# Optimization experiments

Hardware: AMD Instinct MI355X
Metric: run time of the kernel (lower is better)

The kernel has to match this reference:

```python
import jax, jax.numpy as jnp
import numpy as np

N = 100_000          # nodes
E = 3_200_000        # edges (avg degree 32)
EMB = 16             # item embedding dim
IN = EMB + 1         # concat(embed, scalar feature)
HID = 32             # GAT hidden size
NEMB = 1000          # embedding vocab
SLOPE = 0.2          # GATConv leaky_relu negative slope


def setup_inputs() -> dict:
    key = jax.random.key(0)
    ks = jax.random.split(key, 24)
    g = lambda k, shape, fan: jax.random.normal(k, shape, dtype=jnp.float32) * (1.0 / np.sqrt(fan))
    inp = {
        "x_ids": jax.random.randint(ks[0], (N,), 0, NEMB, dtype=jnp.int32),
        "x_feat": jax.random.normal(ks[1], (N, 1), dtype=jnp.float32),
        "src": jax.random.randint(ks[2], (E,), 0, N, dtype=jnp.int32),
        "dst": jax.random.randint(ks[3], (E,), 0, N, dtype=jnp.int32),
        "edge_attr": jax.random.normal(ks[4], (E, 1), dtype=jnp.float32),
        # embedding table
        "emb": g(ks[5], (NEMB, EMB), EMB),
        # GATConv 1 (in=17, out=32, heads=1, edge_dim=1)
        "W1": g(ks[6], (IN, HID), IN),
        "a_s1": g(ks[7], (HID,), HID),
        "a_d1": g(ks[8], (HID,), HID),
        "We1": g(ks[9], (1, HID), 1),
        "a_e1": g(ks[10], (HID,), HID),
        "b1": jnp.zeros((HID,), jnp.float32),
        # GATConv 2 (in=32, out=32)
        "W2": g(ks[11], (HID, HID), HID),
        "a_s2": g(ks[12], (HID,), HID),
        "a_d2": g(ks[13], (HID,), HID),
        "We2": g(ks[14], (1, HID), 1),
        "a_e2": g(ks[15], (HID,), HID),
        "b2": jnp.zeros((HID,), jnp.float32),
        # final linear (32 -> 1)
        "lin_w": g(ks[16], (HID, 1), HID),
        "lin_b": jnp.zeros((1,), jnp.float32),
    }
    return inp


def _gat_conv(x, src, dst, eattr, W, a_s, a_d, We, a_e, b):
    """PyG GATConv (heads=1, concat=True) with edge features, self-loops already added."""
    h = x @ W                                   # [N, HID]
    alpha_src = h @ a_s                         # [N]
    alpha_dst = h @ a_d                         # [N]
    alpha_edge = (eattr @ We) @ a_e             # [E']
    alpha = jax.nn.leaky_relu(alpha_src[src] + alpha_dst[dst] + alpha_edge, SLOPE)
    # segment softmax over incoming edges of each dst node
    m = jax.ops.segment_max(alpha, dst, num_segments=N)
    ex = jnp.exp(alpha - m[dst])
    denom = jax.ops.segment_sum(ex, dst, num_segments=N)
    coef = ex / (denom[dst] + 1e-16)
    out = jax.ops.segment_sum(coef[:, None] * h[src], dst, num_segments=N)
    return out + b


def reference(x_ids, x_feat, src, dst, edge_attr, emb,
              W1, a_s1, a_d1, We1, a_e1, b1,
              W2, a_s2, a_d2, We2, a_e2, b2,
              lin_w, lin_b):
    # embedding lookup + concat scalar feature -> [N, 17]
    x = jnp.concatenate([emb[x_ids], x_feat], axis=1)

    # add self-loops once; self-loop edge_attr = mean of incoming edge attrs (fill_value='mean')
    loop = jnp.arange(N, dtype=src.dtype)
    deg = jax.ops.segment_sum(jnp.ones((E,), x.dtype), dst, num_segments=N)
    loop_attr = jax.ops.segment_sum(edge_attr, dst, num_segments=N) / jnp.maximum(deg, 1.0)[:, None]
    src2 = jnp.concatenate([src, loop])
    dst2 = jnp.concatenate([dst, loop])
    ea2 = jnp.concatenate([edge_attr, loop_attr], axis=0)

    x = _gat_conv(x, src2, dst2, ea2, W1, a_s1, a_d1, We1, a_e1, b1)
    x = jax.nn.relu(x)  # dropout is identity in eval mode
    x = _gat_conv(x, src2, dst2, ea2, W2, a_s2, a_d2, We2, a_e2, b2)
    return x @ lin_w + lin_b  # [N, 1]
```

## Files before the change

### kernel.cpp

```cpp
#include <hip/hip_runtime.h>
#include <hip/hip_fp16.h>

#define NN 100000
#define EE 3200000
#define SLOPE 0.2f

#define BKN 128
constexpr int NBK = (NN + BKN - 1) / BKN;
#define CAP 4544
#define EPB 4096
constexpr int NBB = (EE + EPB - 1) / EPB;
constexpr int NBT = (NN + 255) / 256;
#define SUBN 1344

__global__ void k_fat(const int* __restrict__ src, const int* __restrict__ dst,
                      const float* __restrict__ ea, int* __restrict__ cnt,
                      int2* __restrict__ stage,
                      const int* __restrict__ ids, const float* __restrict__ feat,
                      const float* __restrict__ emb, const float* __restrict__ W,
                      const float* __restrict__ avs, const float* __restrict__ avd,
                      __half* __restrict__ h, float* __restrict__ as_,
                      float* __restrict__ ad_) {
    __shared__ int hst[NBK];
    __shared__ int scl[NBK];
    __shared__ int gdel[NBK];
    __shared__ int aux[256];
    __shared__ int2 rec[EPB];
    __shared__ int addr[EPB];
    int t = threadIdx.x;
    if (blockIdx.x < NBB) {
        int base = blockIdx.x * EPB;
        int nedge = min(EPB, EE - base);
        for (int i = t; i < NBK; i += 256) hst[i] = 0;
        __syncthreads();
        int ds[16], ss[16]; float es[16];
#pragma unroll
        for (int j = 0; j < 16; j++) {
            int e = base + j * 256 + t;
            bool v = e < EE;
            ds[j] = v ? dst[e] : -1;
            ss[j] = v ? src[e] : 0;
            es[j] = v ? ea[e] : 0.f;
            if (v) atomicAdd(&hst[ds[j] >> 7], 1);
        }
        __syncthreads();
        int i0 = t * 4;
        int v0 = (i0 + 0 < NBK) ? hst[i0 + 0] : 0;
        int v1 = (i0 + 1 < NBK) ? hst[i0 + 1] : 0;
        int v2 = (i0 + 2 < NBK) ? hst[i0 + 2] : 0;
        int v3 = (i0 + 3 < NBK) ? hst[i0 + 3] : 0;
        int tsum = v0 + v1 + v2 + v3;
        aux[t] = tsum;
        __syncthreads();
        for (int off = 1; off < 256; off <<= 1) {
            int x = (t >= off) ? aux[t - off] : 0;
            __syncthreads();
            aux[t] += x;
            __syncthreads();
        }
        int ex = aux[t] - tsum;
        if (i0 + 0 < NBK) scl[i0 + 0] = ex;
        if (i0 + 1 < NBK) scl[i0 + 1] = ex + v0;
        if (i0 + 2 < NBK) scl[i0 + 2] = ex + v0 + v1;
        if (i0 + 3 < NBK) scl[i0 + 3] = ex + v0 + v1 + v2;
        __syncthreads();
        for (int i = t; i < NBK; i += 256) {
            int hh = hst[i];
            int g = hh ? atomicAdd(&cnt[i], hh) : 0;
            gdel[i] = (g + i * CAP) - scl[i];
        }
        __syncthreads();
#pragma unroll
        for (int j = 0; j < 16; j++) {
            if (ds[j] >= 0) {
                int bk = ds[j] >> 7;
                int pos = atomicAdd(&scl[bk], 1);
                int gpos = pos + gdel[bk];
                rec[pos] = make_int2(ss[j] | ((ds[j] & 127) << 17), __float_as_int(es[j]));
                addr[pos] = (gpos - bk * CAP < CAP) ? gpos : -1;
            }
        }
        __syncthreads();
        for (int i = t; i < nedge; i += 256) {
            int a = addr[i];
            if (a >= 0) stage[a] = rec[i];
        }
    } else {
        int n = (blockIdx.x - NBB) * 256 + t;
        if (n >= NN) return;
        float hv[32];
#pragma unroll
        for (int j = 0; j < 32; j++) hv[j] = 0.f;
        int id = ids[n];
        const float4* e4 = (const float4*)(emb + (size_t)id * 16);
#pragma unroll
        for (int k4 = 0; k4 < 4; k4++) {
            float4 xv = e4[k4];
            const float* wr = W + k4 * 4 * 32;
#pragma unroll
            for (int j = 0; j < 32; j++)
                hv[j] += xv.x * wr[j] + xv.y * wr[32 + j] + xv.z * wr[64 + j] + xv.w * wr[96 + j];
        }
        float f = feat[n];
#pragma unroll
        for (int j = 0; j < 32; j++) hv[j] += f * W[16 * 32 + j];
        float s = 0.f, d = 0.f;
#pragma unroll
        for (int j = 0; j < 32; j++) { s += hv[j] * avs[j]; d += hv[j] * avd[j]; }
        as_[n] = s;
        ad_[n] = d;
        __half2 tmp[16];
#pragma unroll
        for (int q = 0; q < 16; q++) tmp[q] = __floats2half2_rn(hv[2 * q], hv[2 * q + 1]);
        uint4* dst4 = (uint4*)(h + (size_t)n * 32);
        const uint4* s4 = (const uint4*)tmp;
#pragma unroll
        for (int q = 0; q < 4; q++) dst4[q] = s4[q];
    }
}

template <bool FINAL>
__global__ __launch_bounds__(256, 6) void k_agg(
    const int* __restrict__ cnt, const int2* __restrict__ stage,
    const __half* __restrict__ h, const float* __restrict__ as_,
    const float* __restrict__ ad_, const float* __restrict__ We,
    const float* __restrict__ ae, const float* __restrict__ bias,
    const float* __restrict__ W2, const float* __restrict__ avs2,
    const float* __restrict__ avd2, __half* __restrict__ hout,
    float* __restrict__ as2, float* __restrict__ ad2,
    const float* __restrict__ lw, const float* __restrict__ lb,
    float* __restrict__ out) {
    __shared__ int2 ebuf[SUBN];
    __shared__ int2 xb[4][64];
    __shared__ float w2s[1024];
    __shared__ float xrow[4][32];
    __shared__ int ldeg[32];
    __shared__ float esum[32];
    __shared__ int starts[32];
    __shared__ int lcur[32];
    __shared__ int cnts[32];
    __shared__ float means[32];
    int t = threadIdx.x;
    int b2 = blockIdx.x;
    int b = b2 >> 2, q = b2 & 3;
    int nbase = b * BKN + q * 32;
    int npb = min(32, NN - nbase);
    if (npb <= 0) return;
    int lane = t & 63;
    int wid = t >> 6;
    int g = lane >> 4;
    int cp = (lane & 15) * 2;
    int comp = lane & 31;
    float ce = We[comp] * ae[comp];
#pragma unroll
    for (int off = 1; off < 32; off <<= 1) ce += __shfl_xor(ce, off);

    if (t < 32) { ldeg[t] = 0; esum[t] = 0.f; }
    if (!FINAL)
        for (int i = t; i < 1024; i += 256) w2s[i] = W2[i];
    __syncthreads();
    int c = min(cnt[b], CAP);
    const int2* ep = stage + (size_t)b * CAP;
    for (int i = t; i < c; i += 256) {
        int2 e = ep[i];
        int dl = (e.x >> 17) & 127;
        if ((dl >> 5) == q) {
            atomicAdd(&ldeg[dl & 31], 1);
            atomicAdd(&esum[dl & 31], __int_as_float(e.y));
        }
    }
    __syncthreads();
    if (t < 64) {
        int l = lane;
        int dv = (l < npb) ? ldeg[l] + 1 : 0;
        int v = dv;
#pragma unroll
        for (int off = 1; off < 32; off <<= 1) {
            int x = __shfl_up(v, off);
            if (lane >= off) v += x;
        }
        if (l < 32) {
            int st = v - dv;
            starts[l] = st;
            lcur[l] = st;
            cnts[l] = dv;
            means[l] = esum[l] / fmaxf((float)ldeg[l], 1.0f);
        }
    }
    __syncthreads();
    for (int i = t; i < c; i += 256) {
        int2 e = ep[i];
        int dl = (e.x >> 17) & 127;
        if ((dl >> 5) == q) {
            int pos = atomicAdd(&lcur[dl & 31], 1);
            if (pos < SUBN) ebuf[pos] = make_int2(e.x & 0x1FFFF, e.y);
        }
    }
    __syncthreads();
    if (t < npb) {
        int p = lcur[t];
        if (p < SUBN) ebuf[p] = make_int2(nbase + t, __float_as_int(means[t]));
    }
    __syncthreads();

    for (int i2 = 0; i2 < 8; i2++) {
        int n = wid * 8 + i2;
        if (n >= npb) break;
        int gn = nbase + n;
        int base2 = starts[n];
        int cn = cnts[n];
        if (base2 >= SUBN) cn = 0;
        else if (cn > SUBN - base2) cn = SUBN - base2;
        float adn = ad_[gn];
        float2 acc0 = {0.f, 0.f}, acc1 = {0.f, 0.f}, acc2 = {0.f, 0.f}, acc3 = {0.f, 0.f};
        float exs = 0.f;
        for (int cb = 0; cb < cn; cb += 64) {
            int idx = cb + lane;
            bool val = idx < cn;
            int2 e = ebuf[base2 + (val ? idx : 0)];
            float a = as_[e.x] + adn + ce * __int_as_float(e.y);
            a = (a >= 0.f) ? a : SLOPE * a;
            float ex = val ? __expf(a) : 0.f;
            exs += ex;
            xb[wid][lane] = make_int2(e.x << 5, __float_as_int(ex));
            int m = min(cn - cb, 64);
            for (int j = 0; j < m; j += 16) {
                int2 p0 = xb[wid][j + g];
                int2 p1 = xb[wid][j + 4 + g];
                int2 p2 = xb[wid][j + 8 + g];
                int2 p3 = xb[wid][j + 12 + g];
                float2 h0 = __half22float2(*(const __half2*)(h + p0.x + cp));
                float2 h1 = __half22float2(*(const __half2*)(h + p1.x + cp));
                float2 h2 = __half22float2(*(const __half2*)(h + p2.x + cp));
                float2 h3 = __half22float2(*(const __half2*)(h + p3.x + cp));
                float w0 = __int_as_float(p0.y), w1 = __int_as_float(p1.y);
                float w2 = __int_as_float(p2.y), w3 = __int_as_float(p3.y);
                acc0.x += w0 * h0.x; acc0.y += w0 * h0.y;
                acc1.x += w1 * h1.x; acc1.y += w1 * h1.y;
                acc2.x += w2 * h2.x; acc2.y += w2 * h2.y;
                acc3.x += w3 * h3.x; acc3.y += w3 * h3.y;
            }
        }
        float2 acc;
        acc.x = (acc0.x + acc1.x) + (acc2.x + acc3.x);
        acc.y = (acc0.y + acc1.y) + (acc2.y + acc3.y);
        acc.x += __shfl_xor(acc.x, 16); acc.y += __shfl_xor(acc.y, 16);
        acc.x += __shfl_xor(acc.x, 32); acc.y += __shfl_xor(acc.y, 32);
#pragma unroll
        for (int off = 1; off < 64; off <<= 1) exs += __shfl_xor(exs, off);
        float inv = 1.0f / (exs + 1e-16f);
        float ox = acc.x * inv + bias[cp];
        float oy = acc.y * inv + bias[cp + 1];
        if (FINAL) {
            float y = ox * lw[cp] + oy * lw[cp + 1];
#pragma unroll
            for (int off = 1; off < 16; off <<= 1) y += __shfl_xor(y, off);
            if (lane == 0) out[gn] = y + lb[0];
        } else {
            ox = fmaxf(ox, 0.f);
            oy = fmaxf(oy, 0.f);
            if (lane < 16) { xrow[wid][cp] = ox; xrow[wid][cp + 1] = oy; }
            float hx = 0.f, hy = 0.f;
#pragma unroll
            for (int k = 0; k < 32; k++) {
                float xk = xrow[wid][k];
                hx += xk * w2s[k * 32 + cp];
                hy += xk * w2s[k * 32 + cp + 1];
            }
            float ps = hx * avs2[cp] + hy * avs2[cp + 1];
            float pd = hx * avd2[cp] + hy * avd2[cp + 1];
#pragma unroll
            for (int off = 1; off < 16; off <<= 1) {
                ps += __shfl_xor(ps, off);
                pd += __shfl_xor(pd, off);
            }
            if (lane == 0) { as2[gn] = ps; ad2[gn] = pd; }
            if (lane < 16)
                *(__half2*)(hout + ((size_t)gn << 5) + cp) = __floats2half2_rn(hx, hy);
        }
    }
}


extern "C" void kernel_launch(void* const* d_in, const int* in_sizes, int n_in,
                              void* d_out, int out_size, void* d_ws, size_t ws_size,
                              hipStream_t stream) {
    const int* x_ids = (const int*)d_in[0];
    const float* x_feat = (const float*)d_in[1];
    const int* src = (const int*)d_in[2];
    const int* dst = (const int*)d_in[3];
    const float* eattr = (const float*)d_in[4];
    const float* emb = (const float*)d_in[5];
    const float* W1 = (const float*)d_in[6];
    const float* a_s1 = (const float*)d_in[7];
    const float* a_d1 = (const float*)d_in[8];
    const float* We1 = (const float*)d_in[9];
    const float* a_e1 = (const float*)d_in[10];
    const float* b1 = (const float*)d_in[11];
    const float* W2 = (const float*)d_in[12];
    const float* a_s2 = (const float*)d_in[13];
    const float* a_d2 = (const float*)d_in[14];
    const float* We2 = (const float*)d_in[15];
    const float* a_e2 = (const float*)d_in[16];
    const float* b2 = (const float*)d_in[17];
    const float* lin_w = (const float*)d_in[18];
    const float* lin_b = (const float*)d_in[19];

    char* p = (char*)d_ws;
    auto alloc = [&](size_t bytes) {
        void* r = (void*)p;
        p += (bytes + 255) & ~(size_t)255;
        return r;
    };
    int* cnt = (int*)alloc(NBK * 4);
    float* asb1 = (float*)alloc(NN * 4);
    float* adb1 = (float*)alloc(NN * 4);
    float* asb2 = (float*)alloc(NN * 4);
    float* adb2 = (float*)alloc(NN * 4);
    __half* h1 = (__half*)alloc((size_t)NN * 32 * 2);
    __half* h2 = (__half*)alloc((size_t)NN * 32 * 2);
    int2* stage = (int2*)alloc((size_t)NBK * CAP * 8);
    (void)ws_size; (void)in_sizes; (void)n_in; (void)out_size;

    hipMemsetAsync(cnt, 0, NBK * 4, stream);

    k_fat<<<NBB + NBT, 256, 0, stream>>>(src, dst, eattr, cnt, stage,
                                         x_ids, x_feat, emb, W1, a_s1, a_d1,
                                         h1, asb1, adb1);
    k_agg<false><<<NBK * 4, 256, 0, stream>>>(cnt, stage, h1, asb1, adb1,
                                              We1, a_e1, b1,
                                              W2, a_s2, a_d2, h2, asb2, adb2,
                                              nullptr, nullptr, nullptr);
    k_agg<true><<<NBK * 4, 256, 0, stream>>>(cnt, stage, h2, asb2, adb2,
                                             We2, a_e2, b2,
                                             nullptr, nullptr, nullptr,
                                             nullptr, nullptr, nullptr,
                                             lin_w, lin_b, (float*)d_out);
}
```

Measured before the change: 349.3 us.

## Bucket edges per 32-node sub-block so aggregation reads only its own edges

The edge binning pass now buckets edges by dst>>5 (3125 buckets of 32 nodes) instead of dst>>7. Each aggregation block therefore reads only its own bucket rather than scanning a 128-node bucket four times and discarding three quarters of the entries. The per-block shared histogram grows to 3328 entries and the edges handled per binning block drop to 1792, which means more binning blocks and more global atomics on cnt. Launch bounds are raised to 8 waves, and the code now assumes NN divides evenly by 32 and that each bucket holds at most 1344 edges.

```diff
diff --git a/kernel.cpp b/kernel.cpp
--- a/kernel.cpp
+++ b/kernel.cpp
@@ -5,10 +5,11 @@
 #define EE 3200000
 #define SLOPE 0.2f
 
-#define BKN 128
-constexpr int NBK = (NN + BKN - 1) / BKN;
-#define CAP 4544
-#define EPB 4096
+#define SBN 32
+constexpr int NSB = NN / SBN;
+#define NSBP 3328
+#define CAPS 1344
+#define EPB 1792
 constexpr int NBB = (EE + EPB - 1) / EPB;
 constexpr int NBT = (NN + 255) / 256;
 #define SUBN 1344
@@ -21,9 +22,9 @@
                       const float* __restrict__ avs, const float* __restrict__ avd,
                       __half* __restrict__ h, float* __restrict__ as_,
                       float* __restrict__ ad_) {
-    __shared__ int hst[NBK];
-    __shared__ int scl[NBK];
-    __shared__ int gdel[NBK];
+    __shared__ int hst[NSBP];
+    __shared__ int scl[NSBP];
+    __shared__ int gdel[NSBP];
     __shared__ int aux[256];
     __shared__ int2 rec[EPB];
     __shared__ int addr[EPB];
@@ -31,25 +32,24 @@
     if (blockIdx.x < NBB) {
         int base = blockIdx.x * EPB;
         int nedge = min(EPB, EE - base);
-        for (int i = t; i < NBK; i += 256) hst[i] = 0;
-        __syncthreads();
-        int ds[16], ss[16]; float es[16];
-#pragma unroll
-        for (int j = 0; j < 16; j++) {
+        for (int i = t; i < NSBP; i += 256) hst[i] = 0;
+        __syncthreads();
+        int ds[7], ss[7]; float es[7];
+#pragma unroll
+        for (int j = 0; j < 7; j++) {
             int e = base + j * 256 + t;
             bool v = e < EE;
             ds[j] = v ? dst[e] : -1;
             ss[j] = v ? src[e] : 0;
             es[j] = v ? ea[e] : 0.f;
-            if (v) atomicAdd(&hst[ds[j] >> 7], 1);
-        }
-        __syncthreads();
-        int i0 = t * 4;
-        int v0 = (i0 + 0 < NBK) ? hst[i0 + 0] : 0;
-        int v1 = (i0 + 1 < NBK) ? hst[i0 + 1] : 0;
-        int v2 = (i0 + 2 < NBK) ? hst[i0 + 2] : 0;
-        int v3 = (i0 + 3 < NBK) ? hst[i0 + 3] : 0;
-        int tsum = v0 + v1 + v2 + v3;
+            if (v) atomicAdd(&hst[ds[j] >> 5], 1);
+        }
+        __syncthreads();
+        int i0 = t * 13;
+        int vv[13];
+        int tsum = 0;
+#pragma unroll
+        for (int j = 0; j < 13; j++) { vv[j] = hst[i0 + j]; tsum += vv[j]; }
         aux[t] = tsum;
         __syncthreads();
         for (int off = 1; off < 256; off <<= 1) {
@@ -59,25 +59,23 @@
             __syncthreads();
         }
         int ex = aux[t] - tsum;
-        if (i0 + 0 < NBK) scl[i0 + 0] = ex;
-        if (i0 + 1 < NBK) scl[i0 + 1] = ex + v0;
-        if (i0 + 2 < NBK) scl[i0 + 2] = ex + v0 + v1;
-        if (i0 + 3 < NBK) scl[i0 + 3] = ex + v0 + v1 + v2;
-        __syncthreads();
-        for (int i = t; i < NBK; i += 256) {
+#pragma unroll
+        for (int j = 0; j < 13; j++) { scl[i0 + j] = ex; ex += vv[j]; }
+        __syncthreads();
+        for (int i = t; i < NSB; i += 256) {
             int hh = hst[i];
             int g = hh ? atomicAdd(&cnt[i], hh) : 0;
-            gdel[i] = (g + i * CAP) - scl[i];
-        }
-        __syncthreads();
-#pragma unroll
-        for (int j = 0; j < 16; j++) {
+            gdel[i] = (g + i * CAPS) - scl[i];
+        }
+        __syncthreads();
+#pragma unroll
+        for (int j = 0; j < 7; j++) {
             if (ds[j] >= 0) {
-                int bk = ds[j] >> 7;
+                int bk = ds[j] >> 5;
                 int pos = atomicAdd(&scl[bk], 1);
                 int gpos = pos + gdel[bk];
-                rec[pos] = make_int2(ss[j] | ((ds[j] & 127) << 17), __float_as_int(es[j]));
-                addr[pos] = (gpos - bk * CAP < CAP) ? gpos : -1;
+                rec[pos] = make_int2(ss[j] | ((ds[j] & 31) << 17), __float_as_int(es[j]));
+                addr[pos] = (gpos - bk * CAPS < CAPS) ? gpos : -1;
             }
         }
         __syncthreads();
@@ -120,7 +118,7 @@
 }
 
 template <bool FINAL>
-__global__ __launch_bounds__(256, 6) void k_agg(
+__global__ __launch_bounds__(256, 8) void k_agg(
     const int* __restrict__ cnt, const int2* __restrict__ stage,
     const __half* __restrict__ h, const float* __restrict__ as_,
     const float* __restrict__ ad_, const float* __restrict__ We,
@@ -141,11 +139,8 @@
     __shared__ int cnts[32];
     __shared__ float means[32];
     int t = threadIdx.x;
-    int b2 = blockIdx.x;
-    int b = b2 >> 2, q = b2 & 3;
-    int nbase = b * BKN + q * 32;
-    int npb = min(32, NN - nbase);
-    if (npb <= 0) return;
+    int s = blockIdx.x;
+    int nbase = s * SBN;
     int lane = t & 63;
     int wid = t >> 6;
     int g = lane >> 4;
@@ -159,20 +154,18 @@
     if (!FINAL)
         for (int i = t; i < 1024; i += 256) w2s[i] = W2[i];
     __syncthreads();
-    int c = min(cnt[b], CAP);
-    const int2* ep = stage + (size_t)b * CAP;
+    int c = min(cnt[s], CAPS);
+    const int2* ep = stage + (size_t)s * CAPS;
     for (int i = t; i < c; i += 256) {
         int2 e = ep[i];
-        int dl = (e.x >> 17) & 127;
-        if ((dl >> 5) == q) {
-            atomicAdd(&ldeg[dl & 31], 1);
-            atomicAdd(&esum[dl & 31], __int_as_float(e.y));
-        }
+        int dl = (e.x >> 17) & 31;
+        atomicAdd(&ldeg[dl], 1);
+        atomicAdd(&esum[dl], __int_as_float(e.y));
     }
     __syncthreads();
     if (t < 64) {
         int l = lane;
-        int dv = (l < npb) ? ldeg[l] + 1 : 0;
+        int dv = (l < 32) ? ldeg[l] + 1 : 0;
         int v = dv;
 #pragma unroll
         for (int off = 1; off < 32; off <<= 1) {
@@ -190,14 +183,12 @@
     __syncthreads();
     for (int i = t; i < c; i += 256) {
         int2 e = ep[i];
-        int dl = (e.x >> 17) & 127;
-        if ((dl >> 5) == q) {
-            int pos = atomicAdd(&lcur[dl & 31], 1);
-            if (pos < SUBN) ebuf[pos] = make_int2(e.x & 0x1FFFF, e.y);
-        }
-    }
-    __syncthreads();
-    if (t < npb) {
+        int dl = (e.x >> 17) & 31;
+        int pos = atomicAdd(&lcur[dl], 1);
+        if (pos < SUBN) ebuf[pos] = make_int2(e.x & 0x1FFFF, e.y);
+    }
+    __syncthreads();
+    if (t < 32) {
         int p = lcur[t];
         if (p < SUBN) ebuf[p] = make_int2(nbase + t, __float_as_int(means[t]));
     }
@@ -205,7 +196,6 @@
 
     for (int i2 = 0; i2 < 8; i2++) {
         int n = wid * 8 + i2;
-        if (n >= npb) break;
         int gn = nbase + n;
         int base2 = starts[n];
         int cn = cnts[n];
@@ -312,28 +302,28 @@
         p += (bytes + 255) & ~(size_t)255;
         return r;
     };
-    int* cnt = (int*)alloc(NBK * 4);
+    int* cnt = (int*)alloc(NSB * 4);
     float* asb1 = (float*)alloc(NN * 4);
     float* adb1 = (float*)alloc(NN * 4);
     float* asb2 = (float*)alloc(NN * 4);
     float* adb2 = (float*)alloc(NN * 4);
     __half* h1 = (__half*)alloc((size_t)NN * 32 * 2);
     __half* h2 = (__half*)alloc((size_t)NN * 32 * 2);
-    int2* stage = (int2*)alloc((size_t)NBK * CAP * 8);
+    int2* stage = (int2*)alloc((size_t)NSB * CAPS * 8);
     (void)ws_size; (void)in_sizes; (void)n_in; (void)out_size;
 
-    hipMemsetAsync(cnt, 0, NBK * 4, stream);
+    hipMemsetAsync(cnt, 0, NSB * 4, stream);
 
     k_fat<<<NBB + NBT, 256, 0, stream>>>(src, dst, eattr, cnt, stage,
                                          x_ids, x_feat, emb, W1, a_s1, a_d1,
                                          h1, asb1, adb1);
-    k_agg<false><<<NBK * 4, 256, 0, stream>>>(cnt, stage, h1, asb1, adb1,
-                                              We1, a_e1, b1,
-                                              W2, a_s2, a_d2, h2, asb2, adb2,
-                                              nullptr, nullptr, nullptr);
-    k_agg<true><<<NBK * 4, 256, 0, stream>>>(cnt, stage, h2, asb2, adb2,
-                                             We2, a_e2, b2,
-                                             nullptr, nullptr, nullptr,
-                                             nullptr, nullptr, nullptr,
-                                             lin_w, lin_b, (float*)d_out);
+    k_agg<false><<<NSB, 256, 0, stream>>>(cnt, stage, h1, asb1, adb1,
+                                          We1, a_e1, b1,
+                                          W2, a_s2, a_d2, h2, asb2, adb2,
+                                          nullptr, nullptr, nullptr);
+    k_agg<true><<<NSB, 256, 0, stream>>>(cnt, stage, h2, asb2, adb2,
+                                         We2, a_e2, b2,
+                                         nullptr, nullptr, nullptr,
+                                         nullptr, nullptr, nullptr,
+                                         lin_w, lin_b, (float*)d_out);
 }
```

New measurement: 548.0 us. +56.9%, slower.

## Persist per-node CSR from layer-1 aggregation and reuse it in a warp-per-node layer-2 kernel

Applied to the files above, without the earlier changes.

The layer-1 aggregation kernel now writes its locally built per-subblock edge list (CSR) and per-node offsets to global memory. A new layer-2 kernel assigns one wavefront per node and reads that CSR directly, so it no longer re-scans the staged bucket edges and rebuilds the shared-memory lists a second time. Layer-1 blocks are also launched in an interleaved order, and occupancy launch bounds are raised. The cost is extra global writes for the CSR (about 3.4M int2), and layer-2 loses block-level locality because each wavefront handles a single node, which may leave uneven per-node work.

```diff
diff --git a/kernel.cpp b/kernel.cpp
--- a/kernel.cpp
+++ b/kernel.cpp
@@ -12,6 +12,7 @@
 constexpr int NBB = (EE + EPB - 1) / EPB;
 constexpr int NBT = (NN + 255) / 256;
 #define SUBN 1344
+constexpr int NSB = NBK * 4;
 
 __global__ void k_fat(const int* __restrict__ src, const int* __restrict__ dst,
                       const float* __restrict__ ea, int* __restrict__ cnt,
@@ -119,8 +120,7 @@
     }
 }
 
-template <bool FINAL>
-__global__ __launch_bounds__(256, 6) void k_agg(
+__global__ __launch_bounds__(256, 8) void k_l1(
     const int* __restrict__ cnt, const int2* __restrict__ stage,
     const __half* __restrict__ h, const float* __restrict__ as_,
     const float* __restrict__ ad_, const float* __restrict__ We,
@@ -128,8 +128,7 @@
     const float* __restrict__ W2, const float* __restrict__ avs2,
     const float* __restrict__ avd2, __half* __restrict__ hout,
     float* __restrict__ as2, float* __restrict__ ad2,
-    const float* __restrict__ lw, const float* __restrict__ lb,
-    float* __restrict__ out) {
+    int2* __restrict__ csr, int2* __restrict__ offs2) {
     __shared__ int2 ebuf[SUBN];
     __shared__ int2 xb[4][64];
     __shared__ float w2s[1024];
@@ -141,7 +140,8 @@
     __shared__ int cnts[32];
     __shared__ float means[32];
     int t = threadIdx.x;
-    int b2 = blockIdx.x;
+    int p = blockIdx.x;
+    int b2 = (p & 7) * 391 + (p >> 3);
     int b = b2 >> 2, q = b2 & 3;
     int nbase = b * BKN + q * 32;
     int npb = min(32, NN - nbase);
@@ -156,8 +156,7 @@
     for (int off = 1; off < 32; off <<= 1) ce += __shfl_xor(ce, off);
 
     if (t < 32) { ldeg[t] = 0; esum[t] = 0.f; }
-    if (!FINAL)
-        for (int i = t; i < 1024; i += 256) w2s[i] = W2[i];
+    for (int i = t; i < 1024; i += 256) w2s[i] = W2[i];
     __syncthreads();
     int c = min(cnt[b], CAP);
     const int2* ep = stage + (size_t)b * CAP;
@@ -198,10 +197,20 @@
     }
     __syncthreads();
     if (t < npb) {
-        int p = lcur[t];
-        if (p < SUBN) ebuf[p] = make_int2(nbase + t, __float_as_int(means[t]));
+        int pp = lcur[t];
+        if (pp < SUBN) ebuf[pp] = make_int2(nbase + t, __float_as_int(means[t]));
     }
     __syncthreads();
+    int tot = min(starts[31] + cnts[31], SUBN);
+    int2* cw = csr + (size_t)b2 * SUBN;
+    for (int i = t; i < tot; i += 256) cw[i] = ebuf[i];
+    if (t < npb) {
+        int st = starts[t];
+        int cn = cnts[t];
+        if (st >= SUBN) { st = 0; cn = 0; }
+        else if (cn > SUBN - st) cn = SUBN - st;
+        offs2[nbase + t] = make_int2(b2 * SUBN + st, cn);
+    }
 
     for (int i2 = 0; i2 < 8; i2++) {
         int n = wid * 8 + i2;
@@ -251,34 +260,93 @@
         float inv = 1.0f / (exs + 1e-16f);
         float ox = acc.x * inv + bias[cp];
         float oy = acc.y * inv + bias[cp + 1];
-        if (FINAL) {
-            float y = ox * lw[cp] + oy * lw[cp + 1];
-#pragma unroll
-            for (int off = 1; off < 16; off <<= 1) y += __shfl_xor(y, off);
-            if (lane == 0) out[gn] = y + lb[0];
-        } else {
-            ox = fmaxf(ox, 0.f);
-            oy = fmaxf(oy, 0.f);
-            if (lane < 16) { xrow[wid][cp] = ox; xrow[wid][cp + 1] = oy; }
-            float hx = 0.f, hy = 0.f;
-#pragma unroll
-            for (int k = 0; k < 32; k++) {
-                float xk = xrow[wid][k];
-                hx += xk * w2s[k * 32 + cp];
-                hy += xk * w2s[k * 32 + cp + 1];
-            }
-            float ps = hx * avs2[cp] + hy * avs2[cp + 1];
-            float pd = hx * avd2[cp] + hy * avd2[cp + 1];
-#pragma unroll
-            for (int off = 1; off < 16; off <<= 1) {
-                ps += __shfl_xor(ps, off);
-                pd += __shfl_xor(pd, off);
-            }
-            if (lane == 0) { as2[gn] = ps; ad2[gn] = pd; }
-            if (lane < 16)
-                *(__half2*)(hout + ((size_t)gn << 5) + cp) = __floats2half2_rn(hx, hy);
-        }
-    }
+        ox = fmaxf(ox, 0.f);
+        oy = fmaxf(oy, 0.f);
+        if (lane < 16) { xrow[wid][cp] = ox; xrow[wid][cp + 1] = oy; }
+        float hx = 0.f, hy = 0.f;
+#pragma unroll
+        for (int k = 0; k < 32; k++) {
+            float xk = xrow[wid][k];
+            hx += xk * w2s[k * 32 + cp];
+            hy += xk * w2s[k * 32 + cp + 1];
+        }
+        float ps = hx * avs2[cp] + hy * avs2[cp + 1];
+        float pd = hx * avd2[cp] + hy * avd2[cp + 1];
+#pragma unroll
+        for (int off = 1; off < 16; off <<= 1) {
+            ps += __shfl_xor(ps, off);
+            pd += __shfl_xor(pd, off);
+        }
+        if (lane == 0) { as2[gn] = ps; ad2[gn] = pd; }
+        if (lane < 16)
+            *(__half2*)(hout + ((size_t)gn << 5) + cp) = __floats2half2_rn(hx, hy);
+    }
+}
+
+__global__ void k_gat(const int2* __restrict__ offs2, const int2* __restrict__ csr,
+                      const __half* __restrict__ h, const float* __restrict__ as_,
+                      const float* __restrict__ ad_,
+                      const float* __restrict__ We, const float* __restrict__ ae,
+                      const float* __restrict__ bias,
+                      const float* __restrict__ lw, const float* __restrict__ lb,
+                      float* __restrict__ out) {
+    __shared__ int2 xb[4][64];
+    int wid = threadIdx.x >> 6;
+    int node = blockIdx.x * 4 + wid;
+    int lane = threadIdx.x & 63;
+    int comp = lane & 31;
+    int cp = (lane & 15) * 2;
+    int slot4 = lane >> 4;
+    float c = We[comp] * ae[comp];
+#pragma unroll
+    for (int off = 1; off < 32; off <<= 1) c += __shfl_xor(c, off);
+    int2 oo = offs2[node];
+    int base = oo.x;
+    int cnt = oo.y;
+    float adn = ad_[node];
+    float2 acc0 = {0.f, 0.f}, acc1 = {0.f, 0.f}, acc2 = {0.f, 0.f}, acc3 = {0.f, 0.f};
+    float exs = 0.f;
+    for (int cb = 0; cb < cnt; cb += 64) {
+        int idx = cb + lane;
+        bool val = idx < cnt;
+        int2 e = csr[base + (val ? idx : 0)];
+        float a = as_[e.x] + adn + c * __int_as_float(e.y);
+        a = (a >= 0.f) ? a : SLOPE * a;
+        float ex = val ? __expf(a) : 0.f;
+        exs += ex;
+        xb[wid][lane] = make_int2(e.x << 5, __float_as_int(ex));
+        int m = min(cnt - cb, 64);
+        for (int j = 0; j < m; j += 16) {
+            int2 p0 = xb[wid][j + slot4];
+            int2 p1 = xb[wid][j + 4 + slot4];
+            int2 p2 = xb[wid][j + 8 + slot4];
+            int2 p3 = xb[wid][j + 12 + slot4];
+            float2 h0 = __half22float2(*(const __half2*)(h + p0.x + cp));
+            float2 h1 = __half22float2(*(const __half2*)(h + p1.x + cp));
+            float2 h2 = __half22float2(*(const __half2*)(h + p2.x + cp));
+            float2 h3 = __half22float2(*(const __half2*)(h + p3.x + cp));
+            float w0 = __int_as_float(p0.y), w1 = __int_as_float(p1.y);
+            float w2 = __int_as_float(p2.y), w3 = __int_as_float(p3.y);
+            acc0.x += w0 * h0.x; acc0.y += w0 * h0.y;
+            acc1.x += w1 * h1.x; acc1.y += w1 * h1.y;
+            acc2.x += w2 * h2.x; acc2.y += w2 * h2.y;
+            acc3.x += w3 * h3.x; acc3.y += w3 * h3.y;
+        }
+    }
+    float2 acc;
+    acc.x = (acc0.x + acc1.x) + (acc2.x + acc3.x);
+    acc.y = (acc0.y + acc1.y) + (acc2.y + acc3.y);
+    acc.x += __shfl_xor(acc.x, 16); acc.y += __shfl_xor(acc.y, 16);
+    acc.x += __shfl_xor(acc.x, 32); acc.y += __shfl_xor(acc.y, 32);
+#pragma unroll
+    for (int off = 1; off < 64; off <<= 1) exs += __shfl_xor(exs, off);
+    float inv = 1.0f / (exs + 1e-16f);
+    float ox = acc.x * inv + bias[cp];
+    float oy = acc.y * inv + bias[cp + 1];
+    float y = ox * lw[cp] + oy * lw[cp + 1];
+#pragma unroll
+    for (int off = 1; off < 16; off <<= 1) y += __shfl_xor(y, off);
+    if (lane == 0) out[node] = y + lb[0];
 }
 
 
@@ -313,12 +381,14 @@
         return r;
     };
     int* cnt = (int*)alloc(NBK * 4);
+    int2* offs2 = (int2*)alloc((size_t)NN * 8);
     float* asb1 = (float*)alloc(NN * 4);
     float* adb1 = (float*)alloc(NN * 4);
     float* asb2 = (float*)alloc(NN * 4);
     float* adb2 = (float*)alloc(NN * 4);
     __half* h1 = (__half*)alloc((size_t)NN * 32 * 2);
     __half* h2 = (__half*)alloc((size_t)NN * 32 * 2);
+    int2* csr = (int2*)alloc((size_t)NSB * SUBN * 8);
     int2* stage = (int2*)alloc((size_t)NBK * CAP * 8);
     (void)ws_size; (void)in_sizes; (void)n_in; (void)out_size;
 
@@ -327,13 +397,11 @@
     k_fat<<<NBB + NBT, 256, 0, stream>>>(src, dst, eattr, cnt, stage,
                                          x_ids, x_feat, emb, W1, a_s1, a_d1,
                                          h1, asb1, adb1);
-    k_agg<false><<<NBK * 4, 256, 0, stream>>>(cnt, stage, h1, asb1, adb1,
-                                              We1, a_e1, b1,
-                                              W2, a_s2, a_d2, h2, asb2, adb2,
-                                              nullptr, nullptr, nullptr);
-    k_agg<true><<<NBK * 4, 256, 0, stream>>>(cnt, stage, h2, asb2, adb2,
-                                             We2, a_e2, b2,
-                                             nullptr, nullptr, nullptr,
-                                             nullptr, nullptr, nullptr,
-                                             lin_w, lin_b, (float*)d_out);
+    k_l1<<<NSB, 256, 0, stream>>>(cnt, stage, h1, asb1, adb1,
+                                  We1, a_e1, b1,
+                                  W2, a_s2, a_d2, h2, asb2, adb2,
+                                  csr, offs2);
+    k_gat<<<(NN + 3) / 4, 256, 0, stream>>>(offs2, csr, h2, asb2, adb2,
+                                            We2, a_e2, b2,
+                                            lin_w, lin_b, (float*)d_out);
 }
```

After: 312.2 us. 10.6% less time.
